# Kernel optimization log

Measured on AMD Instinct MI355X. Metric: run time of the kernel, lower is better.

Reference implementation:

```python
import jax, jax.numpy as jnp
import numpy as np
import math

B, M, C = 256, 256, 1024
ALPHA = 0.1

def setup_inputs() -> dict:
    key = jax.random.key(0)
    k1, k2 = jax.random.split(key)
    input_encoded = jax.random.normal(k1, (B, C), dtype=jnp.float32)
    memory_mean = jax.random.normal(k2, (M, C), dtype=jnp.float32)
    return {"input_encoded": input_encoded, "memory_mean": memory_mean}

def reference(input_encoded, memory_mean):
    b, c = input_encoded.shape
    m = memory_mean.shape[0]
    # ---- write_to_memory ----
    # similarity of each input with each prior memory slot: [B, M]
    sims = jnp.einsum('bc,mc->bm', input_encoded, memory_mean)
    closest_idx = jnp.argmax(sims, axis=1)                      # [B]
    sel = memory_mean[closest_idx]                              # [B, C]
    new_row = (1.0 - ALPHA) * sel + ALPHA * input_encoded       # [B, C]
    onehot = (jnp.arange(m)[None, :] == closest_idx[:, None])   # [B, M] bool
    mem = jnp.broadcast_to(memory_mean[None], (b, m, c))
    updated_memory = jnp.where(onehot[:, :, None], new_row[:, None, :], mem)  # [B, M, C]
    dkl_write = 0.5 * jnp.sum((input_encoded - sel) ** 2, axis=1)             # [B]
    # ---- read_with_encoded_input ----
    scale = 1.0 / math.sqrt(c)
    scores = jnp.einsum('bc,bmc->bm', input_encoded, updated_memory) * scale  # [B, M]
    attn = jax.nn.softmax(scores, axis=1)
    z_read = jnp.einsum('bm,bmc->bc', attn, updated_memory)                   # [B, C]
    dkl_read = 0.5 * jnp.sum((z_read - input_encoded) ** 2, axis=1)           # [B]
    kl_div = dkl_write + dkl_read
    return z_read, updated_memory, kl_div
```

## Files before the change

### kernel.cpp

```cpp
#include <hip/hip_runtime.h>
#include <math.h>

#define B_DIM 256
#define M_DIM 256
#define C_DIM 1024
#define C4    256
#define UM_OFF (B_DIM * C_DIM)
#define KL_OFF (UM_OFF + B_DIM * M_DIM * C_DIM)
#define SCALE  0.03125f

__device__ __forceinline__ float dot4(float4 a, float4 b) {
    return a.x*b.x + a.y*b.y + a.z*b.z + a.w*b.w;
}
__device__ __forceinline__ float wsum(float v) {
    #pragma unroll
    for (int off = 32; off; off >>= 1) v += __shfl_xor(v, off, 64);
    return v;
}
__device__ __forceinline__ float wmax(float v) {
    #pragma unroll
    for (int off = 32; off; off >>= 1) v = fmaxf(v, __shfl_xor(v, off, 64));
    return v;
}
__device__ __forceinline__ float4 blend9(float4 v, float4 xr) {
    return make_float4(0.9f*v.x + 0.1f*xr.x, 0.9f*v.y + 0.1f*xr.y,
                       0.9f*v.z + 0.1f*xr.z, 0.9f*v.w + 0.1f*xr.w);
}

__global__ __launch_bounds__(1024) void tm_pre(const float* __restrict__ x,
                                               const float* __restrict__ mem,
                                               float* __restrict__ out,
                                               int* __restrict__ idx_ws) {
    const int b = blockIdx.x;
    const int t = threadIdx.x;
    const int lane = t & 63;
    const int wv = t >> 6;
    const int tc = t & 255;
    const int q  = t >> 8;

    __shared__ float4 s_x[C4];
    __shared__ float4 s_zp[3][C4];
    __shared__ float  s_sims[M_DIM];
    __shared__ float  s_w[4];

    const float4* mem4 = (const float4*)mem;

    float4 xv = make_float4(0.f, 0.f, 0.f, 0.f);
    if (q == 0) {
        xv = ((const float4*)(x + (size_t)b * C_DIM))[tc];
        s_x[tc] = xv;
    }
    __syncthreads();

    {
        const float4 xr0 = s_x[lane];
        const float4 xr1 = s_x[lane + 64];
        const float4 xr2 = s_x[lane + 128];
        const float4 xr3 = s_x[lane + 192];
        #pragma unroll 4
        for (int i = 0; i < 16; ++i) {
            const int m = (wv << 4) | i;
            const float4* mr = mem4 + (m << 8);
            float acc = dot4(mr[lane],     xr0) + dot4(mr[lane+64],  xr1)
                      + dot4(mr[lane+128], xr2) + dot4(mr[lane+192], xr3);
            acc = wsum(acc);
            if (lane == 0) s_sims[m] = acc;
        }
    }
    __syncthreads();

    const float v0 = s_sims[lane];
    const float v1 = s_sims[lane + 64];
    const float v2 = s_sims[lane + 128];
    const float v3 = s_sims[lane + 192];
    const float4 xa = s_x[lane], xb = s_x[lane + 64];
    const float4 xc = s_x[lane + 128], xd = s_x[lane + 192];
    const float n2 = wsum(dot4(xa,xa) + dot4(xb,xb) + dot4(xc,xc) + dot4(xd,xd));

    float av = v0; int am = lane;
    if (v1 > av) { av = v1; am = lane + 64; }
    if (v2 > av) { av = v2; am = lane + 128; }
    if (v3 > av) { av = v3; am = lane + 192; }
    #pragma unroll
    for (int off = 32; off; off >>= 1) {
        float ov = __shfl_xor(av, off, 64);
        int   oi = __shfl_xor(am, off, 64);
        if (ov > av || (ov == av && oi < am)) { av = ov; am = oi; }
    }
    const int idx = am;
    if (t == 0) idx_ws[b] = idx;
    const float fused = 0.9f * av + 0.1f * n2;

    float s0 = ((lane      ) == idx ? fused : v0) * SCALE;
    float s1 = ((lane +  64) == idx ? fused : v1) * SCALE;
    float s2 = ((lane + 128) == idx ? fused : v2) * SCALE;
    float s3 = ((lane + 192) == idx ? fused : v3) * SCALE;
    const float mx = wmax(fmaxf(fmaxf(s0, s1), fmaxf(s2, s3)));
    const float e0 = expf(s0 - mx), e1 = expf(s1 - mx);
    const float e2 = expf(s2 - mx), e3 = expf(s3 - mx);
    const float inv = 1.0f / wsum(e0 + e1 + e2 + e3);
    const float a0 = e0 * inv, a1 = e1 * inv, a2 = e2 * inv, a3 = e3 * inv;

    float aidx;
    if      (idx <  64) aidx = __shfl(a0, idx,       64);
    else if (idx < 128) aidx = __shfl(a1, idx - 64,  64);
    else if (idx < 192) aidx = __shfl(a2, idx - 128, 64);
    else                aidx = __shfl(a3, idx - 192, 64);
    aidx *= 0.1f;

    float dw = 0.f;
    if (wv == 0) {
        const float4* ir = mem4 + (idx << 8);
        float4 q0 = ir[lane], q1 = ir[lane+64], q2 = ir[lane+128], q3 = ir[lane+192];
        float p = 0.f; float4 dq;
        dq = make_float4(xa.x-q0.x, xa.y-q0.y, xa.z-q0.z, xa.w-q0.w); p += dot4(dq,dq);
        dq = make_float4(xb.x-q1.x, xb.y-q1.y, xb.z-q1.z, xb.w-q1.w); p += dot4(dq,dq);
        dq = make_float4(xc.x-q2.x, xc.y-q2.y, xc.z-q2.z, xc.w-q2.w); p += dot4(dq,dq);
        dq = make_float4(xd.x-q3.x, xd.y-q3.y, xd.z-q3.z, xd.w-q3.w); p += dot4(dq,dq);
        dw = wsum(p);
    }

    float4 z = make_float4(0.f, 0.f, 0.f, 0.f);
    {
        const float4* zsrc = mem4 + ((q << 6) << 8) + tc;
        auto zrun = [&](float areg) {
            #pragma unroll 4
            for (int i = 0; i < 64; ++i) {
                const float a = __shfl(areg, i, 64);
                float4 v = zsrc[i << 8];
                z.x = fmaf(a, v.x, z.x);
                z.y = fmaf(a, v.y, z.y);
                z.z = fmaf(a, v.z, z.z);
                z.w = fmaf(a, v.w, z.w);
            }
        };
        if      (q == 0) zrun(a0);
        else if (q == 1) zrun(a1);
        else if (q == 2) zrun(a2);
        else             zrun(a3);
    }
    if (q) s_zp[q - 1][tc] = z;
    __syncthreads();
    float drp = 0.f;
    if (q == 0) {
        float4 z1 = s_zp[0][tc], z2 = s_zp[1][tc], z3 = s_zp[2][tc];
        z.x += z1.x + z2.x + z3.x;
        z.y += z1.y + z2.y + z3.y;
        z.z += z1.z + z2.z + z3.z;
        z.w += z1.w + z2.w + z3.w;
        float4 sl = mem4[(idx << 8) + tc];
        float4 d = make_float4(xv.x - sl.x, xv.y - sl.y, xv.z - sl.z, xv.w - sl.w);
        z.x = fmaf(aidx, d.x, z.x);
        z.y = fmaf(aidx, d.y, z.y);
        z.z = fmaf(aidx, d.z, z.z);
        z.w = fmaf(aidx, d.w, z.w);
        float ex = z.x - xv.x, ey = z.y - xv.y, ez = z.z - xv.z, ew = z.w - xv.w;
        drp = ex*ex + ey*ey + ez*ez + ew*ew;
        ((float4*)out)[(size_t)b * C4 + tc] = z;
    }
    {
        float s = wsum(drp);
        if (q == 0 && lane == 0) s_w[wv] = s;
    }
    __syncthreads();
    if (t == 0) out[KL_OFF + b] = 0.5f * (dw + s_w[0] + s_w[1] + s_w[2] + s_w[3]);
}

__global__ __launch_bounds__(256) void tm_stream(const float* __restrict__ x,
                                                 const float* __restrict__ mem,
                                                 const int* __restrict__ idx_ws,
                                                 float* __restrict__ out_um) {
    const int j = blockIdx.x;
    const int b  = j >> 5;
    const int m0 = (j & 31) << 3;
    const int t = threadIdx.x;

    const float4* src = (const float4*)mem + (m0 << 8) + t;
    float4 r0 = src[0 << 8];
    float4 r1 = src[1 << 8];
    float4 r2 = src[2 << 8];
    float4 r3 = src[3 << 8];
    float4 r4 = src[4 << 8];
    float4 r5 = src[5 << 8];
    float4 r6 = src[6 << 8];
    float4 r7 = src[7 << 8];

    const int li = idx_ws[b] - m0;
    if (li >= 0 && li < 8) {
        float4 xv = ((const float4*)(x + (size_t)b * C_DIM))[t];
        if (li == 0) r0 = blend9(r0, xv);
        if (li == 1) r1 = blend9(r1, xv);
        if (li == 2) r2 = blend9(r2, xv);
        if (li == 3) r3 = blend9(r3, xv);
        if (li == 4) r4 = blend9(r4, xv);
        if (li == 5) r5 = blend9(r5, xv);
        if (li == 6) r6 = blend9(r6, xv);
        if (li == 7) r7 = blend9(r7, xv);
    }

    float4* dst = (float4*)out_um + ((size_t)b << 16) + (m0 << 8) + t;
    dst[0 << 8] = r0;
    dst[1 << 8] = r1;
    dst[2 << 8] = r2;
    dst[3 << 8] = r3;
    dst[4 << 8] = r4;
    dst[5 << 8] = r5;
    dst[6 << 8] = r6;
    dst[7 << 8] = r7;
}

extern "C" void kernel_launch(void* const* d_in, const int* in_sizes, int n_in,
                              void* d_out, int out_size, void* d_ws, size_t ws_size,
                              hipStream_t stream) {
    const float* x   = (const float*)d_in[0];
    const float* mem = (const float*)d_in[1];
    float* out = (float*)d_out;
    int* idx_ws = (int*)d_ws;

    tm_pre<<<dim3(B_DIM), dim3(1024), 0, stream>>>(x, mem, out, idx_ws);
    tm_stream<<<dim3(8192), dim3(256), 0, stream>>>(x, mem, idx_ws, out + UM_OFF);
}
```

Baseline: 67.48 us.

## Merge compute and broadcast-copy into one launch, patch selected rows afterward

The attention/argmax blocks and the 256 MB memory-broadcast copy blocks now run in a single grid, so the copy no longer waits for argmax. A small follow-up kernel overwrites each batch's selected row with the blended value. The compute blocks shrink from 1024 to 256 threads and keep the full M loop per thread for z_read, reading attention weights from shared memory. The risk is that compute blocks become slower, and that the selected rows are written twice.

```diff
diff --git a/kernel.cpp b/kernel.cpp
--- a/kernel.cpp
+++ b/kernel.cpp
@@ -27,45 +27,64 @@
                        0.9f*v.z + 0.1f*xr.z, 0.9f*v.w + 0.1f*xr.w);
 }
 
-__global__ __launch_bounds__(1024) void tm_pre(const float* __restrict__ x,
+__global__ __launch_bounds__(256) void tm_main(const float* __restrict__ x,
                                                const float* __restrict__ mem,
                                                float* __restrict__ out,
                                                int* __restrict__ idx_ws) {
-    const int b = blockIdx.x;
+    const int bid = blockIdx.x;
     const int t = threadIdx.x;
+    const float4* mem4 = (const float4*)mem;
+
+    if (bid >= B_DIM) {
+        const int j  = bid - B_DIM;
+        const int b  = j >> 5;
+        const int m0 = (j & 31) << 3;
+        const float4* src = mem4 + (m0 << 8) + t;
+        float4 r0 = src[0 << 8];
+        float4 r1 = src[1 << 8];
+        float4 r2 = src[2 << 8];
+        float4 r3 = src[3 << 8];
+        float4 r4 = src[4 << 8];
+        float4 r5 = src[5 << 8];
+        float4 r6 = src[6 << 8];
+        float4 r7 = src[7 << 8];
+        float4* dst = (float4*)(out + UM_OFF) + ((size_t)b << 16) + (m0 << 8) + t;
+        dst[0 << 8] = r0;
+        dst[1 << 8] = r1;
+        dst[2 << 8] = r2;
+        dst[3 << 8] = r3;
+        dst[4 << 8] = r4;
+        dst[5 << 8] = r5;
+        dst[6 << 8] = r6;
+        dst[7 << 8] = r7;
+        return;
+    }
+
+    const int b = bid;
     const int lane = t & 63;
     const int wv = t >> 6;
-    const int tc = t & 255;
-    const int q  = t >> 8;
 
     __shared__ float4 s_x[C4];
-    __shared__ float4 s_zp[3][C4];
     __shared__ float  s_sims[M_DIM];
-    __shared__ float  s_w[4];
+    __shared__ float  s_attn[M_DIM];
+    __shared__ float  s_w0[4], s_w1[4];
 
-    const float4* mem4 = (const float4*)mem;
-
-    float4 xv = make_float4(0.f, 0.f, 0.f, 0.f);
-    if (q == 0) {
-        xv = ((const float4*)(x + (size_t)b * C_DIM))[tc];
-        s_x[tc] = xv;
-    }
+    float4 xv = ((const float4*)(x + (size_t)b * C_DIM))[t];
+    s_x[t] = xv;
     __syncthreads();
 
-    {
-        const float4 xr0 = s_x[lane];
-        const float4 xr1 = s_x[lane + 64];
-        const float4 xr2 = s_x[lane + 128];
-        const float4 xr3 = s_x[lane + 192];
-        #pragma unroll 4
-        for (int i = 0; i < 16; ++i) {
-            const int m = (wv << 4) | i;
-            const float4* mr = mem4 + (m << 8);
-            float acc = dot4(mr[lane],     xr0) + dot4(mr[lane+64],  xr1)
-                      + dot4(mr[lane+128], xr2) + dot4(mr[lane+192], xr3);
-            acc = wsum(acc);
-            if (lane == 0) s_sims[m] = acc;
-        }
+    const float4 xr0 = s_x[lane];
+    const float4 xr1 = s_x[lane + 64];
+    const float4 xr2 = s_x[lane + 128];
+    const float4 xr3 = s_x[lane + 192];
+    #pragma unroll 4
+    for (int i = 0; i < 64; ++i) {
+        const int m = (wv << 6) | i;
+        const float4* mr = mem4 + (m << 8);
+        float acc = dot4(mr[lane],     xr0) + dot4(mr[lane+64],  xr1)
+                  + dot4(mr[lane+128], xr2) + dot4(mr[lane+192], xr3);
+        acc = wsum(acc);
+        if (lane == 0) s_sims[m] = acc;
     }
     __syncthreads();
 
@@ -73,9 +92,7 @@
     const float v1 = s_sims[lane + 64];
     const float v2 = s_sims[lane + 128];
     const float v3 = s_sims[lane + 192];
-    const float4 xa = s_x[lane], xb = s_x[lane + 64];
-    const float4 xc = s_x[lane + 128], xd = s_x[lane + 192];
-    const float n2 = wsum(dot4(xa,xa) + dot4(xb,xb) + dot4(xc,xc) + dot4(xd,xd));
+    const float n2 = wsum(dot4(xr0,xr0) + dot4(xr1,xr1) + dot4(xr2,xr2) + dot4(xr3,xr3));
 
     float av = v0; int am = lane;
     if (v1 > av) { av = v1; am = lane + 64; }
@@ -101,112 +118,61 @@
     const float inv = 1.0f / wsum(e0 + e1 + e2 + e3);
     const float a0 = e0 * inv, a1 = e1 * inv, a2 = e2 * inv, a3 = e3 * inv;
 
+    if (wv == 0) {
+        s_attn[lane]       = a0;
+        s_attn[lane + 64]  = a1;
+        s_attn[lane + 128] = a2;
+        s_attn[lane + 192] = a3;
+    }
+
     float aidx;
     if      (idx <  64) aidx = __shfl(a0, idx,       64);
     else if (idx < 128) aidx = __shfl(a1, idx - 64,  64);
     else if (idx < 192) aidx = __shfl(a2, idx - 128, 64);
     else                aidx = __shfl(a3, idx - 192, 64);
     aidx *= 0.1f;
-
-    float dw = 0.f;
-    if (wv == 0) {
-        const float4* ir = mem4 + (idx << 8);
-        float4 q0 = ir[lane], q1 = ir[lane+64], q2 = ir[lane+128], q3 = ir[lane+192];
-        float p = 0.f; float4 dq;
-        dq = make_float4(xa.x-q0.x, xa.y-q0.y, xa.z-q0.z, xa.w-q0.w); p += dot4(dq,dq);
-        dq = make_float4(xb.x-q1.x, xb.y-q1.y, xb.z-q1.z, xb.w-q1.w); p += dot4(dq,dq);
-        dq = make_float4(xc.x-q2.x, xc.y-q2.y, xc.z-q2.z, xc.w-q2.w); p += dot4(dq,dq);
-        dq = make_float4(xd.x-q3.x, xd.y-q3.y, xd.z-q3.z, xd.w-q3.w); p += dot4(dq,dq);
-        dw = wsum(p);
-    }
+    __syncthreads();
 
     float4 z = make_float4(0.f, 0.f, 0.f, 0.f);
-    {
-        const float4* zsrc = mem4 + ((q << 6) << 8) + tc;
-        auto zrun = [&](float areg) {
-            #pragma unroll 4
-            for (int i = 0; i < 64; ++i) {
-                const float a = __shfl(areg, i, 64);
-                float4 v = zsrc[i << 8];
-                z.x = fmaf(a, v.x, z.x);
-                z.y = fmaf(a, v.y, z.y);
-                z.z = fmaf(a, v.z, z.z);
-                z.w = fmaf(a, v.w, z.w);
-            }
-        };
-        if      (q == 0) zrun(a0);
-        else if (q == 1) zrun(a1);
-        else if (q == 2) zrun(a2);
-        else             zrun(a3);
+    #pragma unroll 8
+    for (int m = 0; m < M_DIM; ++m) {
+        const float a = s_attn[m];
+        float4 v = mem4[(m << 8) + t];
+        z.x = fmaf(a, v.x, z.x);
+        z.y = fmaf(a, v.y, z.y);
+        z.z = fmaf(a, v.z, z.z);
+        z.w = fmaf(a, v.w, z.w);
     }
-    if (q) s_zp[q - 1][tc] = z;
+    float4 sl = mem4[(idx << 8) + t];
+    float4 d = make_float4(xv.x - sl.x, xv.y - sl.y, xv.z - sl.z, xv.w - sl.w);
+    const float dwp = dot4(d, d);
+    z.x = fmaf(aidx, d.x, z.x);
+    z.y = fmaf(aidx, d.y, z.y);
+    z.z = fmaf(aidx, d.z, z.z);
+    z.w = fmaf(aidx, d.w, z.w);
+    float ex = z.x - xv.x, ey = z.y - xv.y, ez = z.z - xv.z, ew = z.w - xv.w;
+    const float drp = ex*ex + ey*ey + ez*ez + ew*ew;
+    ((float4*)out)[(size_t)b * C4 + t] = z;
+
+    const float sw = wsum(dwp);
+    const float sr = wsum(drp);
+    if (lane == 0) { s_w0[wv] = sw; s_w1[wv] = sr; }
     __syncthreads();
-    float drp = 0.f;
-    if (q == 0) {
-        float4 z1 = s_zp[0][tc], z2 = s_zp[1][tc], z3 = s_zp[2][tc];
-        z.x += z1.x + z2.x + z3.x;
-        z.y += z1.y + z2.y + z3.y;
-        z.z += z1.z + z2.z + z3.z;
-        z.w += z1.w + z2.w + z3.w;
-        float4 sl = mem4[(idx << 8) + tc];
-        float4 d = make_float4(xv.x - sl.x, xv.y - sl.y, xv.z - sl.z, xv.w - sl.w);
-        z.x = fmaf(aidx, d.x, z.x);
-        z.y = fmaf(aidx, d.y, z.y);
-        z.z = fmaf(aidx, d.z, z.z);
-        z.w = fmaf(aidx, d.w, z.w);
-        float ex = z.x - xv.x, ey = z.y - xv.y, ez = z.z - xv.z, ew = z.w - xv.w;
-        drp = ex*ex + ey*ey + ez*ez + ew*ew;
-        ((float4*)out)[(size_t)b * C4 + tc] = z;
-    }
-    {
-        float s = wsum(drp);
-        if (q == 0 && lane == 0) s_w[wv] = s;
-    }
-    __syncthreads();
-    if (t == 0) out[KL_OFF + b] = 0.5f * (dw + s_w[0] + s_w[1] + s_w[2] + s_w[3]);
+    if (t == 0)
+        out[KL_OFF + b] = 0.5f * (s_w0[0]+s_w0[1]+s_w0[2]+s_w0[3]
+                                + s_w1[0]+s_w1[1]+s_w1[2]+s_w1[3]);
 }
 
-__global__ __launch_bounds__(256) void tm_stream(const float* __restrict__ x,
-                                                 const float* __restrict__ mem,
-                                                 const int* __restrict__ idx_ws,
-                                                 float* __restrict__ out_um) {
-    const int j = blockIdx.x;
-    const int b  = j >> 5;
-    const int m0 = (j & 31) << 3;
+__global__ __launch_bounds__(256) void tm_fix(const float* __restrict__ x,
+                                              const float* __restrict__ mem,
+                                              const int* __restrict__ idx_ws,
+                                              float* __restrict__ out_um) {
+    const int b = blockIdx.x;
     const int t = threadIdx.x;
-
-    const float4* src = (const float4*)mem + (m0 << 8) + t;
-    float4 r0 = src[0 << 8];
-    float4 r1 = src[1 << 8];
-    float4 r2 = src[2 << 8];
-    float4 r3 = src[3 << 8];
-    float4 r4 = src[4 << 8];
-    float4 r5 = src[5 << 8];
-    float4 r6 = src[6 << 8];
-    float4 r7 = src[7 << 8];
-
-    const int li = idx_ws[b] - m0;
-    if (li >= 0 && li < 8) {
-        float4 xv = ((const float4*)(x + (size_t)b * C_DIM))[t];
-        if (li == 0) r0 = blend9(r0, xv);
-        if (li == 1) r1 = blend9(r1, xv);
-        if (li == 2) r2 = blend9(r2, xv);
-        if (li == 3) r3 = blend9(r3, xv);
-        if (li == 4) r4 = blend9(r4, xv);
-        if (li == 5) r5 = blend9(r5, xv);
-        if (li == 6) r6 = blend9(r6, xv);
-        if (li == 7) r7 = blend9(r7, xv);
-    }
-
-    float4* dst = (float4*)out_um + ((size_t)b << 16) + (m0 << 8) + t;
-    dst[0 << 8] = r0;
-    dst[1 << 8] = r1;
-    dst[2 << 8] = r2;
-    dst[3 << 8] = r3;
-    dst[4 << 8] = r4;
-    dst[5 << 8] = r5;
-    dst[6 << 8] = r6;
-    dst[7 << 8] = r7;
+    const int idx = idx_ws[b];
+    float4 sl = ((const float4*)mem)[(idx << 8) + t];
+    float4 xv = ((const float4*)(x + (size_t)b * C_DIM))[t];
+    ((float4*)out_um)[((size_t)b << 16) + (idx << 8) + t] = blend9(sl, xv);
 }
 
 extern "C" void kernel_launch(void* const* d_in, const int* in_sizes, int n_in,
@@ -217,6 +183,6 @@
     float* out = (float*)d_out;
     int* idx_ws = (int*)d_ws;
 
-    tm_pre<<<dim3(B_DIM), dim3(1024), 0, stream>>>(x, mem, out, idx_ws);
-    tm_stream<<<dim3(8192), dim3(256), 0, stream>>>(x, mem, idx_ws, out + UM_OFF);
+    tm_main<<<dim3(B_DIM + 8192), dim3(256), 0, stream>>>(x, mem, out, idx_ws);
+    tm_fix<<<dim3(B_DIM), dim3(256), 0, stream>>>(x, mem, idx_ws, out + UM_OFF);
 }
```

After: 69.49 us. +3.0%, slower.

## Fuse similarity computation into memory streaming kernel and reorder launches

Applied to the files above, without the earlier changes.

Computes input-memory similarities inside the streaming copy kernel, which already holds the memory rows in registers, and stores them in the z_read output region as scratch. The post kernel reads these similarities instead of recomputing the full dot-product pass. It then writes the blended row over the copied updated memory. This removes a full matrix-vector pass per batch row but adds wave reductions and a shared-memory sync to the bandwidth-bound streaming kernel.

```diff
diff --git a/kernel.cpp b/kernel.cpp
--- a/kernel.cpp
+++ b/kernel.cpp
@@ -27,10 +27,55 @@
                        0.9f*v.z + 0.1f*xr.z, 0.9f*v.w + 0.1f*xr.w);
 }
 
-__global__ __launch_bounds__(1024) void tm_pre(const float* __restrict__ x,
-                                               const float* __restrict__ mem,
-                                               float* __restrict__ out,
-                                               int* __restrict__ idx_ws) {
+__global__ __launch_bounds__(256) void tm_stream(const float* __restrict__ x,
+                                                 const float* __restrict__ mem,
+                                                 float* __restrict__ out) {
+    const int j = blockIdx.x;
+    const int b  = j >> 5;
+    const int m0 = (j & 31) << 3;
+    const int t = threadIdx.x;
+    const int lane = t & 63;
+    const int wv = t >> 6;
+
+    __shared__ float s_p[8][4];
+
+    const float4* src = (const float4*)mem + (m0 << 8) + t;
+    float4 r0 = src[0 << 8];
+    float4 r1 = src[1 << 8];
+    float4 r2 = src[2 << 8];
+    float4 r3 = src[3 << 8];
+    float4 r4 = src[4 << 8];
+    float4 r5 = src[5 << 8];
+    float4 r6 = src[6 << 8];
+    float4 r7 = src[7 << 8];
+    const float4 xv = ((const float4*)(x + (size_t)b * C_DIM))[t];
+
+    float p0 = dot4(r0, xv), p1 = dot4(r1, xv), p2 = dot4(r2, xv), p3 = dot4(r3, xv);
+    float p4 = dot4(r4, xv), p5 = dot4(r5, xv), p6 = dot4(r6, xv), p7 = dot4(r7, xv);
+    p0 = wsum(p0); p1 = wsum(p1); p2 = wsum(p2); p3 = wsum(p3);
+    p4 = wsum(p4); p5 = wsum(p5); p6 = wsum(p6); p7 = wsum(p7);
+    if (lane == 0) {
+        s_p[0][wv] = p0; s_p[1][wv] = p1; s_p[2][wv] = p2; s_p[3][wv] = p3;
+        s_p[4][wv] = p4; s_p[5][wv] = p5; s_p[6][wv] = p6; s_p[7][wv] = p7;
+    }
+    __syncthreads();
+    if (t < 8)
+        out[(size_t)b * C_DIM + m0 + t] = s_p[t][0] + s_p[t][1] + s_p[t][2] + s_p[t][3];
+
+    float4* dst = (float4*)(out + UM_OFF) + ((size_t)b << 16) + (m0 << 8) + t;
+    dst[0 << 8] = r0;
+    dst[1 << 8] = r1;
+    dst[2 << 8] = r2;
+    dst[3 << 8] = r3;
+    dst[4 << 8] = r4;
+    dst[5 << 8] = r5;
+    dst[6 << 8] = r6;
+    dst[7 << 8] = r7;
+}
+
+__global__ __launch_bounds__(1024) void tm_post(const float* __restrict__ x,
+                                                const float* __restrict__ mem,
+                                                float* __restrict__ out) {
     const int b = blockIdx.x;
     const int t = threadIdx.x;
     const int lane = t & 63;
@@ -40,7 +85,6 @@
 
     __shared__ float4 s_x[C4];
     __shared__ float4 s_zp[3][C4];
-    __shared__ float  s_sims[M_DIM];
     __shared__ float  s_w[4];
 
     const float4* mem4 = (const float4*)mem;
@@ -52,27 +96,11 @@
     }
     __syncthreads();
 
-    {
-        const float4 xr0 = s_x[lane];
-        const float4 xr1 = s_x[lane + 64];
-        const float4 xr2 = s_x[lane + 128];
-        const float4 xr3 = s_x[lane + 192];
-        #pragma unroll 4
-        for (int i = 0; i < 16; ++i) {
-            const int m = (wv << 4) | i;
-            const float4* mr = mem4 + (m << 8);
-            float acc = dot4(mr[lane],     xr0) + dot4(mr[lane+64],  xr1)
-                      + dot4(mr[lane+128], xr2) + dot4(mr[lane+192], xr3);
-            acc = wsum(acc);
-            if (lane == 0) s_sims[m] = acc;
-        }
-    }
-    __syncthreads();
-
-    const float v0 = s_sims[lane];
-    const float v1 = s_sims[lane + 64];
-    const float v2 = s_sims[lane + 128];
-    const float v3 = s_sims[lane + 192];
+    const float* simsrow = out + (size_t)b * C_DIM;
+    const float v0 = simsrow[lane];
+    const float v1 = simsrow[lane + 64];
+    const float v2 = simsrow[lane + 128];
+    const float v3 = simsrow[lane + 192];
     const float4 xa = s_x[lane], xb = s_x[lane + 64];
     const float4 xc = s_x[lane + 128], xd = s_x[lane + 192];
     const float n2 = wsum(dot4(xa,xa) + dot4(xb,xb) + dot4(xc,xc) + dot4(xd,xd));
@@ -88,7 +116,6 @@
         if (ov > av || (ov == av && oi < am)) { av = ov; am = oi; }
     }
     const int idx = am;
-    if (t == 0) idx_ws[b] = idx;
     const float fused = 0.9f * av + 0.1f * n2;
 
     float s0 = ((lane      ) == idx ? fused : v0) * SCALE;
@@ -157,6 +184,7 @@
         float ex = z.x - xv.x, ey = z.y - xv.y, ez = z.z - xv.z, ew = z.w - xv.w;
         drp = ex*ex + ey*ey + ez*ez + ew*ew;
         ((float4*)out)[(size_t)b * C4 + tc] = z;
+        ((float4*)(out + UM_OFF))[((size_t)b << 16) + (idx << 8) + tc] = blend9(sl, xv);
     }
     {
         float s = wsum(drp);
@@ -164,49 +192,6 @@
     }
     __syncthreads();
     if (t == 0) out[KL_OFF + b] = 0.5f * (dw + s_w[0] + s_w[1] + s_w[2] + s_w[3]);
-}
-
-__global__ __launch_bounds__(256) void tm_stream(const float* __restrict__ x,
-                                                 const float* __restrict__ mem,
-                                                 const int* __restrict__ idx_ws,
-                                                 float* __restrict__ out_um) {
-    const int j = blockIdx.x;
-    const int b  = j >> 5;
-    const int m0 = (j & 31) << 3;
-    const int t = threadIdx.x;
-
-    const float4* src = (const float4*)mem + (m0 << 8) + t;
-    float4 r0 = src[0 << 8];
-    float4 r1 = src[1 << 8];
-    float4 r2 = src[2 << 8];
-    float4 r3 = src[3 << 8];
-    float4 r4 = src[4 << 8];
-    float4 r5 = src[5 << 8];
-    float4 r6 = src[6 << 8];
-    float4 r7 = src[7 << 8];
-
-    const int li = idx_ws[b] - m0;
-    if (li >= 0 && li < 8) {
-        float4 xv = ((const float4*)(x + (size_t)b * C_DIM))[t];
-        if (li == 0) r0 = blend9(r0, xv);
-        if (li == 1) r1 = blend9(r1, xv);
-        if (li == 2) r2 = blend9(r2, xv);
-        if (li == 3) r3 = blend9(r3, xv);
-        if (li == 4) r4 = blend9(r4, xv);
-        if (li == 5) r5 = blend9(r5, xv);
-        if (li == 6) r6 = blend9(r6, xv);
-        if (li == 7) r7 = blend9(r7, xv);
-    }
-
-    float4* dst = (float4*)out_um + ((size_t)b << 16) + (m0 << 8) + t;
-    dst[0 << 8] = r0;
-    dst[1 << 8] = r1;
-    dst[2 << 8] = r2;
-    dst[3 << 8] = r3;
-    dst[4 << 8] = r4;
-    dst[5 << 8] = r5;
-    dst[6 << 8] = r6;
-    dst[7 << 8] = r7;
 }
 
 extern "C" void kernel_launch(void* const* d_in, const int* in_sizes, int n_in,
@@ -215,8 +200,7 @@
     const float* x   = (const float*)d_in[0];
     const float* mem = (const float*)d_in[1];
     float* out = (float*)d_out;
-    int* idx_ws = (int*)d_ws;
-
-    tm_pre<<<dim3(B_DIM), dim3(1024), 0, stream>>>(x, mem, out, idx_ws);
-    tm_stream<<<dim3(8192), dim3(256), 0, stream>>>(x, mem, idx_ws, out + UM_OFF);
-}
+
+    tm_stream<<<dim3(8192), dim3(256), 0, stream>>>(x, mem, out);
+    tm_post<<<dim3(B_DIM), dim3(1024), 0, stream>>>(x, mem, out);
+}
```

Measured after the change: 60.14 us. -10.9%, faster.
